# Optimization experiments

Measured on AMD Instinct MI355X. Metric: run time of the kernel, lower is better.

The kernel has to match this reference:

```python
import jax, jax.numpy as jnp
import numpy as np

DIM, DIM_K, DIM_U, HEADS, SCOPE = 256, 16, 1, 4, 23
DIM_V = DIM // HEADS  # 64
EPS = 1e-5


def _bn(x, gamma, beta):
    # training-mode BatchNorm2d over (b, h, w), biased variance, per-channel affine
    mean = jnp.mean(x, axis=(0, 2, 3), keepdims=True)
    var = jnp.var(x, axis=(0, 2, 3), keepdims=True)
    xhat = (x - mean) * jax.lax.rsqrt(var + EPS)
    return xhat * gamma[None, :, None, None] + beta[None, :, None, None]


def setup_inputs() -> dict:
    key = jax.random.key(0)
    ks = jax.random.split(key, 8)
    c_out = HEADS * DIM_K + DIM_K * DIM_U + DIM_V * DIM_U  # 144
    x = jax.random.normal(ks[0], (16, DIM, 64, 64), dtype=jnp.float32)
    w_qkv = jax.random.normal(ks[1], (c_out, DIM), dtype=jnp.float32) * (1.0 / np.sqrt(DIM))
    gamma_q = jnp.ones((HEADS * DIM_K,), jnp.float32)
    beta_q = jnp.zeros((HEADS * DIM_K,), jnp.float32)
    gamma_v = jnp.ones((DIM_V * DIM_U,), jnp.float32)
    beta_v = jnp.zeros((DIM_V * DIM_U,), jnp.float32)
    fan_in = DIM_U * SCOPE * SCOPE
    w_lconv = jax.random.normal(ks[2], (DIM_K, DIM_U, 1, SCOPE, SCOPE), dtype=jnp.float32) * (1.0 / np.sqrt(fan_in))
    b_lconv = jnp.zeros((DIM_K,), jnp.float32)
    return {"x": x, "w_qkv": w_qkv, "gamma_q": gamma_q, "beta_q": beta_q,
            "gamma_v": gamma_v, "beta_v": beta_v, "w_lconv": w_lconv, "b_lconv": b_lconv}


def reference(x, w_qkv, gamma_q, beta_q, gamma_v, beta_v, w_lconv, b_lconv):
    b, c, h, w = x.shape
    m = h * w
    # 1x1 conv projection
    qkv = jnp.einsum('oc,bchw->bohw', w_qkv, x)
    q = qkv[:, :HEADS * DIM_K]
    k = qkv[:, HEADS * DIM_K:HEADS * DIM_K + DIM_K * DIM_U]
    v = qkv[:, HEADS * DIM_K + DIM_K * DIM_U:]
    # q: 'b (k n) h w -> b n k m'
    q = _bn(q, gamma_q, beta_q).reshape(b, DIM_K, HEADS, m).transpose(0, 2, 1, 3)
    # v: 'b (v u) h w -> b u v m'
    v = _bn(v, gamma_v, beta_v).reshape(b, DIM_V, DIM_U, m).transpose(0, 2, 1, 3)
    # k: 'b (u k) h w -> b u k m', softmax over m
    k = jax.nn.softmax(k.reshape(b, DIM_U, DIM_K, m), axis=-1)
    content_lambda = jnp.einsum('bukm,buvm->bkv', k, v)
    # position lambda: Conv3d over (v, h, w) with kernel (1, scope, scope)
    v5 = v.reshape(b, DIM_U, DIM_V, h, w)
    pad = (SCOPE - 1) // 2
    pl = jax.lax.conv_general_dilated(
        v5, w_lconv, window_strides=(1, 1, 1),
        padding=[(0, 0), (pad, pad), (pad, pad)],
        dimension_numbers=('NCDHW', 'OIDHW', 'NCDHW'))
    pl = pl + b_lconv[None, :, None, None, None]
    position_lambda = pl.reshape(b, DIM_K, DIM_V, m)
    content_output = jnp.einsum('bnkm,bkv->bnvm', q, content_lambda)
    position_output = jnp.einsum('bnkm,bkvm->bnvm', q, position_lambda)
    out = (content_output + position_output).reshape(b, HEADS * DIM_V, h, w)
    return out
```

## Files before the change

### kernel.cpp

```cpp
#include <hip/hip_runtime.h>
#include <math.h>

#define NB    16
#define CDIM  256
#define COUT  144
#define MPIX  4096
#define SCOPE 23
#define PADH  11
#define BNEPS 1e-5f

typedef __attribute__((ext_vector_type(4))) float f32x4;
typedef __attribute__((ext_vector_type(8))) short s16x8;

__device__ __forceinline__ unsigned short f2bf(float f) {
    unsigned u = __builtin_bit_cast(unsigned, f);
    unsigned r = (u + 0x7FFFu + ((u >> 16) & 1u)) >> 16;
    return (unsigned short)r;
}

__global__ void prep_frags(const float* __restrict__ w, const float* __restrict__ wl,
                           short* __restrict__ wqf, short* __restrict__ wfrag) {
    int i = blockIdx.x * 256 + threadIdx.x;
    if (i < 36864) {
        int j = i & 7, lane = (i >> 3) & 63;
        int fi = i >> 9;
        int mf = fi % 9, kc = fi / 9;
        int o = mf * 16 + (lane & 15);
        int c = kc * 32 + (lane >> 4) * 8 + j;
        wqf[i] = (short)f2bf(w[o * 256 + c]);
        return;
    }
    int i2 = i - 36864;
    if (i2 < 23 * 64 * 8) {
        int j = i2 & 7, l = (i2 >> 3) & 63, dy = i2 >> 9;
        int k = l & 15, t = ((l >> 4) << 3) + j;
        float wv = (t < SCOPE) ? wl[k * 529 + dy * 23 + t] : 0.f;
        wfrag[i2] = (short)f2bf(wv);
    }
}

__global__ void __launch_bounds__(256, 4) gemm_qkv(const float* __restrict__ x,
                                                   const short* __restrict__ wqf,
                                                   float* __restrict__ qkv,
                                                   float* __restrict__ statpart,
                                                   float* __restrict__ kpart) {
    __shared__ unsigned pk[16 * 65];
    __shared__ float ssum[4][144], ssq[4][144];
    __shared__ float sse[4][16];
    int mt = blockIdx.x, b = blockIdx.y;
    int m0 = mt * 64;
    int tid = threadIdx.x;
    int px64 = tid & 63, c2b = tid >> 6;
    int lane = tid & 63, wv = tid >> 6;
    int pxl = lane & 15, kgq = lane >> 4;
    const float* xb = x + (size_t)b * CDIM * MPIX;
    float* qtb = qkv + (size_t)b * COUT * MPIX;
    const s16x8* wfv = (const s16x8*)wqf;

    f32x4 acc[9];
#pragma unroll
    for (int mf = 0; mf < 9; mf++) acc[mf] = 0.f;

#pragma unroll 1
    for (int kc = 0; kc < 8; kc++) {
        if (kc > 0) __syncthreads();
#pragma unroll
        for (int it = 0; it < 4; it++) {
            int c2 = c2b + it * 4;
            float x0 = xb[(size_t)(kc * 32 + 2 * c2) * MPIX + m0 + px64];
            float x1 = xb[(size_t)(kc * 32 + 2 * c2 + 1) * MPIX + m0 + px64];
            pk[c2 * 65 + px64] = (unsigned)f2bf(x0) | ((unsigned)f2bf(x1) << 16);
        }
        __syncthreads();
        const unsigned* bp = &pk[kgq * 4 * 65 + wv * 16 + pxl];
        int4 bi = make_int4(bp[0], bp[65], bp[130], bp[195]);
        s16x8 bf = __builtin_bit_cast(s16x8, bi);
#pragma unroll
        for (int mf = 0; mf < 9; mf++) {
            s16x8 af = wfv[(kc * 9 + mf) * 64 + lane];
            acc[mf] = __builtin_amdgcn_mfma_f32_16x16x32_bf16(af, bf, acc[mf], 0, 0, 0);
        }
    }

    int m = m0 + wv * 16 + pxl;
#pragma unroll
    for (int mf = 0; mf < 9; mf++) {
#pragma unroll
        for (int r = 0; r < 4; r++) {
            int o = mf * 16 + kgq * 4 + r;
            if (mf < 4) qtb[(size_t)m * 64 + o] = acc[mf][r];
            else qkv[((size_t)b * COUT + o) * MPIX + m] = acc[mf][r];
        }
    }

#pragma unroll
    for (int mf = 0; mf < 9; mf++) {
#pragma unroll
        for (int r = 0; r < 4; r++) {
            float s = acc[mf][r];
            float s2 = s * s;
#pragma unroll
            for (int off = 1; off < 16; off <<= 1) {
                s += __shfl_xor(s, off);
                s2 += __shfl_xor(s2, off);
            }
            if (mf == 4) {
                float e = __expf(acc[mf][r]);
#pragma unroll
                for (int off = 1; off < 16; off <<= 1) e += __shfl_xor(e, off);
                if (pxl == 0) sse[wv][kgq * 4 + r] = e;
            }
            if (pxl == 0) {
                int ch = mf * 16 + kgq * 4 + r;
                ssum[wv][ch] = s;
                ssq[wv][ch] = s2;
            }
        }
    }
    __syncthreads();
    if (tid < 144) {
        float s = ssum[0][tid] + ssum[1][tid] + ssum[2][tid] + ssum[3][tid];
        float s2 = ssq[0][tid] + ssq[1][tid] + ssq[2][tid] + ssq[3][tid];
        size_t idx = (((size_t)tid * 16 + b) * 64 + mt) * 2;
        statpart[idx + 0] = s;
        statpart[idx + 1] = s2;
    }
    if (tid >= 144 && tid < 160) {
        int kc = tid - 144;
        float e = sse[0][kc] + sse[1][kc] + sse[2][kc] + sse[3][kc];
        kpart[((size_t)kc * 16 + b) * 64 + mt] = e;
    }
}

__global__ void stats_finalize(const float* __restrict__ statpart,
                               const float* __restrict__ kpart,
                               const float* __restrict__ gq, const float* __restrict__ bq,
                               const float* __restrict__ gv, const float* __restrict__ bv,
                               float* __restrict__ ascale, float* __restrict__ dshift,
                               float* __restrict__ ksm) {
    int tid = threadIdx.x;
    if (blockIdx.x >= 128) {
        int id = blockIdx.x - 128;
        if (tid < 64) {
            float s = kpart[(size_t)id * 64 + tid];
#pragma unroll
            for (int off = 32; off > 0; off >>= 1) s += __shfl_down(s, off);
            if (tid == 0) ksm[id] = 1.0f / s;
        }
        return;
    }
    int sch = blockIdx.x;
    int gch = (sch < 64) ? sch : sch + 16;
    const float* sp = statpart + (size_t)gch * 1024 * 2;
    float s = 0.f, s2 = 0.f;
    for (int i = tid; i < 1024; i += 256) {
        s += sp[i * 2 + 0];
        s2 += sp[i * 2 + 1];
    }
#pragma unroll
    for (int off = 32; off > 0; off >>= 1) {
        s += __shfl_down(s, off);
        s2 += __shfl_down(s2, off);
    }
    __shared__ float red[8];
    int wid = tid >> 6, lane = tid & 63;
    if (lane == 0) { red[wid * 2] = s; red[wid * 2 + 1] = s2; }
    __syncthreads();
    if (tid == 0) {
        float ts = 0.f, ts2 = 0.f;
#pragma unroll
        for (int w2 = 0; w2 < 4; w2++) { ts += red[w2 * 2]; ts2 += red[w2 * 2 + 1]; }
        const float invN = 1.0f / 65536.0f;
        float mean = ts * invN;
        float var = ts2 * invN - mean * mean;
        float g = (sch < 64) ? gq[sch] : gv[sch - 64];
        float be = (sch < 64) ? bq[sch] : bv[sch - 64];
        float a = g * rsqrtf(var + BNEPS);
        ascale[sch] = a;
        dshift[sch] = be - mean * a;
    }
}

__global__ void cl_partial(const float* __restrict__ qkv, const float* __restrict__ ksm,
                           const float* __restrict__ ascale, const float* __restrict__ dshift,
                           float* __restrict__ clpart) {
    __shared__ float vsT[128][65];
    __shared__ float pk2[16][132];
    __shared__ float skr[16];
    int mc = blockIdx.x, b = blockIdx.y;
    int m0 = mc * 256;
    int tid = threadIdx.x;
    int vc = tid & 63, kg = tid >> 6;
    if (tid < 16) skr[tid] = ksm[(size_t)tid * 16 + b];
    float acc[4] = {0.f, 0.f, 0.f, 0.f};
    for (int half = 0; half < 2; half++) {
        int mh = m0 + half * 128;
        __syncthreads();
        for (int i = tid; i < 64 * 128; i += 256) {
            int r = i >> 7, c = i & 127;
            vsT[c][r] = fmaf(ascale[64 + r], qkv[((size_t)b * COUT + 80 + r) * MPIX + mh + c],
                             dshift[64 + r]);
        }
        for (int i = tid; i < 16 * 128; i += 256) {
            int kc = i >> 7, mm = i & 127;
            pk2[kc][mm] = __expf(qkv[((size_t)b * COUT + 64 + kc) * MPIX + mh + mm]) * skr[kc];
        }
        __syncthreads();
        for (int mm = 0; mm < 128; mm++) {
            float vv = vsT[mm][vc];
#pragma unroll
            for (int i = 0; i < 4; i++) {
                int kc = kg * 4 + i;
                acc[i] = fmaf(pk2[kc][mm], vv, acc[i]);
            }
        }
    }
#pragma unroll
    for (int i = 0; i < 4; i++) {
        int kc = kg * 4 + i;
        clpart[(((size_t)b * 16 + mc) * 16 + kc) * 64 + vc] = acc[i];
    }
}

__global__ void cl_reduce(const float* __restrict__ clpart, float* __restrict__ cl) {
    int b = blockIdx.x;
    for (int o = threadIdx.x; o < 1024; o += 256) {
        float s = 0.f;
        for (int mc = 0; mc < 16; mc++)
            s += clpart[((size_t)b * 16 + mc) * 1024 + o];
        cl[(size_t)b * 1024 + o] = s;
    }
}

__global__ void __launch_bounds__(256) bnq_t(float* __restrict__ qkv,
                                             const float* __restrict__ ascale,
                                             const float* __restrict__ dshift) {
    __shared__ float sv[64][65];
    int mt = blockIdx.x, b = blockIdx.y;
    int m0 = mt * 64;
    float* qb = qkv + (size_t)b * COUT * MPIX;
    int tid = threadIdx.x;
    int c = tid & 63, mg = tid >> 6;
    float a = ascale[c], d = dshift[c];
#pragma unroll
    for (int i = 0; i < 16; i++) {
        int m = mg * 16 + i;
        sv[m][c] = fmaf(a, qb[(size_t)(m0 + m) * 64 + c], d);
    }
    __syncthreads();
    int m = tid >> 2, jb = (tid & 3) * 8;
    unsigned dw[8];
#pragma unroll
    for (int j = 0; j < 8; j++) {
        int cc = jb * 2 + 2 * j;
        dw[j] = (unsigned)f2bf(sv[m][cc]) | ((unsigned)f2bf(sv[m][cc + 1]) << 16);
    }
    unsigned* dst = (unsigned*)qb + (size_t)(m0 + m) * 64 + jb;
    *(uint4*)dst = make_uint4(dw[0], dw[1], dw[2], dw[3]);
    *(uint4*)(dst + 4) = make_uint4(dw[4], dw[5], dw[6], dw[7]);
}

#define SPW 88
#define LD_FRAG(P) __builtin_bit_cast(s16x8, make_int4((P)[0], (P)[2], (P)[4], (P)[6]))
#define STEP(DY, J) do {                                                        \
    const unsigned* pnew_ = xbase + ((DY) + 3) * SPW;                           \
    rw[((J) + 3) & 3][0] = LD_FRAG(pnew_);                                      \
    rw[((J) + 3) & 3][1] = LD_FRAG(pnew_ + 16);                                 \
    int dyn_ = ((DY) + 3 < 22) ? (DY) + 3 : 22;                                 \
    wr[((J) + 3) & 3] = wf[dyn_ * 64 + lane];                                   \
    _Pragma("unroll")                                                           \
    for (int ty_ = 0; ty_ < 4; ty_++) {                                         \
      _Pragma("unroll")                                                         \
      for (int x2_ = 0; x2_ < 2; x2_++) {                                       \
        int t_ = ty_ * 2 + x2_;                                                 \
        acc[t_] = __builtin_amdgcn_mfma_f32_16x16x32_bf16(                      \
            wr[(J) & 3], rw[((J) + ty_) & 3][x2_], acc[t_], 0, 0, 0);           \
      }                                                                         \
    }                                                                           \
  } while (0)

__global__ void __launch_bounds__(256, 4) lambda_main(
    const float* __restrict__ qkv, const float* __restrict__ ascale,
    const float* __restrict__ dshift, const float* __restrict__ cl,
    const short* __restrict__ wfrag, const float* __restrict__ bl,
    float* __restrict__ out) {
    __shared__ unsigned spack[54 * SPW + 8];
    __shared__ float sck[16];

    int vc = blockIdx.x, b = blockIdx.y, h = blockIdx.z;
    int tid = threadIdx.x;

    if (tid < 16) sck[tid] = cl[((size_t)b * 16 + tid) * 64 + vc] + bl[tid];

    float av = ascale[64 + vc], dv = dshift[64 + vc];
    const float* vrow = qkv + ((size_t)b * COUT + 80 + vc) * MPIX;
    for (int i = tid; i < 54 * SPW; i += 256) {
        int y = i / SPW, e = i - y * SPW;
        int iy = h * 32 + y - PADH;
        float f0 = 0.f, f1 = 0.f;
        if ((unsigned)iy < 64u) {
            int ix0 = e - PADH, ix1 = e - PADH + 1;
            if ((unsigned)ix0 < 64u) f0 = fmaf(av, vrow[iy * 64 + ix0], dv);
            if ((unsigned)ix1 < 64u) f1 = fmaf(av, vrow[iy * 64 + ix1], dv);
        }
        spack[i] = (unsigned)f2bf(f0) | ((unsigned)f2bf(f1) << 16);
    }
    if (tid < 8) spack[54 * SPW + tid] = 0u;
    __syncthreads();

    int lane = tid & 63;
    int wv = tid >> 6;
    int px = lane & 15;
    int kg = lane >> 4;
    const s16x8* wf = (const s16x8*)wfrag;

    const unsigned* qtb = (const unsigned*)(qkv + (size_t)b * COUT * MPIX);
    float* ob = out + (size_t)b * 256 * MPIX;

    float sck_l[4];
#pragma unroll
    for (int r = 0; r < 4; r++) sck_l[r] = sck[kg * 4 + r];

#pragma unroll 1
    for (int gg = 0; gg < 2; gg++) {
        int y0 = (gg * 4 + wv) * 4;
        const unsigned* base = &spack[y0 * SPW + px + kg * 8];

#pragma unroll 1
        for (int xh = 0; xh < 2; xh++) {
            const unsigned* xbase = base + xh * 32;
            f32x4 acc[8];
#pragma unroll
            for (int t = 0; t < 8; t++) acc[t] = 0.f;

            s16x8 rw[4][2];
            s16x8 wr[4];
#pragma unroll
            for (int r0 = 0; r0 < 3; r0++) {
                const unsigned* p = xbase + r0 * SPW;
                rw[r0][0] = LD_FRAG(p);
                rw[r0][1] = LD_FRAG(p + 16);
            }
#pragma unroll
            for (int s = 0; s < 3; s++) wr[s] = wf[s * 64 + lane];

#pragma unroll 1
            for (int i8 = 0; i8 < 2; i8++) {
                int dyb = i8 * 8;
                STEP(dyb + 0, 0);
                STEP(dyb + 1, 1);
                STEP(dyb + 2, 2);
                STEP(dyb + 3, 3);
                STEP(dyb + 4, 4);
                STEP(dyb + 5, 5);
                STEP(dyb + 6, 6);
                STEP(dyb + 7, 7);
            }
            STEP(16, 0);
            STEP(17, 1);
            STEP(18, 2);
            STEP(19, 3);
            STEP(20, 4);
            STEP(21, 5);
            STEP(22, 6);

#pragma unroll
            for (int t = 0; t < 8; t++) {
                int ty = t >> 1, x2 = t & 1;
                int m0 = (h * 32 + y0 + ty) * 64 + (xh * 2 + x2) * 16;
                float lam[4];
#pragma unroll
                for (int r = 0; r < 4; r++) lam[r] = acc[t][r] + sck_l[r];
                const unsigned* qp = &qtb[(size_t)(m0 + px) * 64 + kg * 8];
                uint4 qa = *(const uint4*)qp;
                uint4 qb4 = *(const uint4*)(qp + 4);
                unsigned dws[8] = {qa.x, qa.y, qa.z, qa.w, qb4.x, qb4.y, qb4.z, qb4.w};
                float po[4] = {0.f, 0.f, 0.f, 0.f};
#pragma unroll
                for (int d = 0; d < 8; d++) {
                    float q0 = __builtin_bit_cast(float, dws[d] << 16);
                    float q1 = __builtin_bit_cast(float, dws[d] & 0xffff0000u);
                    int i0 = 2 * d, i1 = 2 * d + 1;
                    po[i0 & 3] = fmaf(q0, lam[i0 >> 2], po[i0 & 3]);
                    po[i1 & 3] = fmaf(q1, lam[i1 >> 2], po[i1 & 3]);
                }
#pragma unroll
                for (int n = 0; n < 4; n++) {
                    po[n] += __shfl_xor(po[n], 16);
                    po[n] += __shfl_xor(po[n], 32);
                }
                float sv = (kg == 0) ? po[0] : (kg == 1) ? po[1] : (kg == 2) ? po[2] : po[3];
                ob[(size_t)(kg * 64 + vc) * MPIX + m0 + px] = sv;
            }
        }
    }
}

extern "C" void kernel_launch(void* const* d_in, const int* in_sizes, int n_in,
                              void* d_out, int out_size, void* d_ws, size_t ws_size,
                              hipStream_t stream) {
    const float* x      = (const float*)d_in[0];
    const float* w_qkv  = (const float*)d_in[1];
    const float* gq     = (const float*)d_in[2];
    const float* bq     = (const float*)d_in[3];
    const float* gv     = (const float*)d_in[4];
    const float* bv     = (const float*)d_in[5];
    const float* wl     = (const float*)d_in[6];
    const float* bl     = (const float*)d_in[7];
    float* out = (float*)d_out;

    float* ws     = (float*)d_ws;
    float* qkv    = ws;
    float* ascale = qkv + 9437184;
    float* dshift = ascale + 128;
    float* clpart = dshift + 128;
    float* clb    = clpart + 262144;
    short* wfrag  = (short*)(clb + 16384);
    short* wqf    = (short*)(clb + 16384 + 5888 + 64);
    float* statpart = (float*)(wqf + 36864);
    float* kpart  = statpart + 294912;
    float* ksm    = kpart + 16384;

    prep_frags<<<190, 256, 0, stream>>>(w_qkv, wl, wqf, wfrag);
    gemm_qkv<<<dim3(64, 16), 256, 0, stream>>>(x, wqf, qkv, statpart, kpart);
    stats_finalize<<<384, 256, 0, stream>>>(statpart, kpart, gq, bq, gv, bv,
                                            ascale, dshift, ksm);
    cl_partial<<<dim3(16, 16), 256, 0, stream>>>(qkv, ksm, ascale, dshift, clpart);
    cl_reduce<<<16, 256, 0, stream>>>(clpart, clb);
    bnq_t<<<dim3(64, 16), 256, 0, stream>>>(qkv, ascale, dshift);
    lambda_main<<<dim3(64, 16, 2), 256, 0, stream>>>(qkv, ascale, dshift, clb, wfrag, bl, out);
}
```

Before: 200.6 us.

## Merge content-lambda partials and q transform into one launch, fold reduce into main

Combines the cl_partial and bnq_t kernels into a single launch whose blocks take one of two roles by blockIdx.x, so the two independent jobs run concurrently. It also removes the cl_reduce kernel by having lambda_main sum the 16 partials directly when it loads the content lambda. This cuts two kernel launches and their serialization gaps. In exchange, each lambda_main block does a small redundant 16-way reduction, and the smem footprint for the q-transform blocks is now the larger union size.

```diff
diff --git a/kernel.cpp b/kernel.cpp
--- a/kernel.cpp
+++ b/kernel.cpp
@@ -181,15 +181,46 @@
     }
 }
 
-__global__ void cl_partial(const float* __restrict__ qkv, const float* __restrict__ ksm,
-                           const float* __restrict__ ascale, const float* __restrict__ dshift,
-                           float* __restrict__ clpart) {
-    __shared__ float vsT[128][65];
-    __shared__ float pk2[16][132];
-    __shared__ float skr[16];
-    int mc = blockIdx.x, b = blockIdx.y;
+__global__ void __launch_bounds__(256) cl_bnq(float* __restrict__ qkv,
+                                              const float* __restrict__ ksm,
+                                              const float* __restrict__ ascale,
+                                              const float* __restrict__ dshift,
+                                              float* __restrict__ clpart) {
+    __shared__ float smem[128 * 65 + 16 * 132 + 16];
+    int role = blockIdx.x, b = blockIdx.y;
+    int tid = threadIdx.x;
+
+    if (role >= 16) {
+        float (*sv)[65] = (float(*)[65])smem;
+        int mt = role - 16;
+        int m0 = mt * 64;
+        float* qb = qkv + (size_t)b * COUT * MPIX;
+        int c = tid & 63, mg = tid >> 6;
+        float a = ascale[c], d = dshift[c];
+#pragma unroll
+        for (int i = 0; i < 16; i++) {
+            int m = mg * 16 + i;
+            sv[m][c] = fmaf(a, qb[(size_t)(m0 + m) * 64 + c], d);
+        }
+        __syncthreads();
+        int m = tid >> 2, jb = (tid & 3) * 8;
+        unsigned dw[8];
+#pragma unroll
+        for (int j = 0; j < 8; j++) {
+            int cc = jb * 2 + 2 * j;
+            dw[j] = (unsigned)f2bf(sv[m][cc]) | ((unsigned)f2bf(sv[m][cc + 1]) << 16);
+        }
+        unsigned* dst = (unsigned*)qb + (size_t)(m0 + m) * 64 + jb;
+        *(uint4*)dst = make_uint4(dw[0], dw[1], dw[2], dw[3]);
+        *(uint4*)(dst + 4) = make_uint4(dw[4], dw[5], dw[6], dw[7]);
+        return;
+    }
+
+    float (*vsT)[65] = (float(*)[65])smem;
+    float (*pk2)[132] = (float(*)[132])(smem + 128 * 65);
+    float* skr = smem + 128 * 65 + 16 * 132;
+    int mc = role;
     int m0 = mc * 256;
-    int tid = threadIdx.x;
     int vc = tid & 63, kg = tid >> 6;
     if (tid < 16) skr[tid] = ksm[(size_t)tid * 16 + b];
     float acc[4] = {0.f, 0.f, 0.f, 0.f};
@@ -220,44 +251,6 @@
         int kc = kg * 4 + i;
         clpart[(((size_t)b * 16 + mc) * 16 + kc) * 64 + vc] = acc[i];
     }
-}
-
-__global__ void cl_reduce(const float* __restrict__ clpart, float* __restrict__ cl) {
-    int b = blockIdx.x;
-    for (int o = threadIdx.x; o < 1024; o += 256) {
-        float s = 0.f;
-        for (int mc = 0; mc < 16; mc++)
-            s += clpart[((size_t)b * 16 + mc) * 1024 + o];
-        cl[(size_t)b * 1024 + o] = s;
-    }
-}
-
-__global__ void __launch_bounds__(256) bnq_t(float* __restrict__ qkv,
-                                             const float* __restrict__ ascale,
-                                             const float* __restrict__ dshift) {
-    __shared__ float sv[64][65];
-    int mt = blockIdx.x, b = blockIdx.y;
-    int m0 = mt * 64;
-    float* qb = qkv + (size_t)b * COUT * MPIX;
-    int tid = threadIdx.x;
-    int c = tid & 63, mg = tid >> 6;
-    float a = ascale[c], d = dshift[c];
-#pragma unroll
-    for (int i = 0; i < 16; i++) {
-        int m = mg * 16 + i;
-        sv[m][c] = fmaf(a, qb[(size_t)(m0 + m) * 64 + c], d);
-    }
-    __syncthreads();
-    int m = tid >> 2, jb = (tid & 3) * 8;
-    unsigned dw[8];
-#pragma unroll
-    for (int j = 0; j < 8; j++) {
-        int cc = jb * 2 + 2 * j;
-        dw[j] = (unsigned)f2bf(sv[m][cc]) | ((unsigned)f2bf(sv[m][cc + 1]) << 16);
-    }
-    unsigned* dst = (unsigned*)qb + (size_t)(m0 + m) * 64 + jb;
-    *(uint4*)dst = make_uint4(dw[0], dw[1], dw[2], dw[3]);
-    *(uint4*)(dst + 4) = make_uint4(dw[4], dw[5], dw[6], dw[7]);
 }
 
 #define SPW 88
@@ -281,7 +274,7 @@
 
 __global__ void __launch_bounds__(256, 4) lambda_main(
     const float* __restrict__ qkv, const float* __restrict__ ascale,
-    const float* __restrict__ dshift, const float* __restrict__ cl,
+    const float* __restrict__ dshift, const float* __restrict__ clpart,
     const short* __restrict__ wfrag, const float* __restrict__ bl,
     float* __restrict__ out) {
     __shared__ unsigned spack[54 * SPW + 8];
@@ -290,7 +283,12 @@
     int vc = blockIdx.x, b = blockIdx.y, h = blockIdx.z;
     int tid = threadIdx.x;
 
-    if (tid < 16) sck[tid] = cl[((size_t)b * 16 + tid) * 64 + vc] + bl[tid];
+    if (tid < 16) {
+        float s = 0.f;
+        for (int mc2 = 0; mc2 < 16; mc2++)
+            s += clpart[(((size_t)b * 16 + mc2) * 16 + tid) * 64 + vc];
+        sck[tid] = s + bl[tid];
+    }
 
     float av = ascale[64 + vc], dv = dshift[64 + vc];
     const float* vrow = qkv + ((size_t)b * COUT + 80 + vc) * MPIX;
@@ -414,9 +412,8 @@
     float* ascale = qkv + 9437184;
     float* dshift = ascale + 128;
     float* clpart = dshift + 128;
-    float* clb    = clpart + 262144;
-    short* wfrag  = (short*)(clb + 16384);
-    short* wqf    = (short*)(clb + 16384 + 5888 + 64);
+    short* wfrag  = (short*)(clpart + 262144);
+    short* wqf    = (short*)(clpart + 262144 + 5888 + 64);
     float* statpart = (float*)(wqf + 36864);
     float* kpart  = statpart + 294912;
     float* ksm    = kpart + 16384;
@@ -425,8 +422,6 @@
     gemm_qkv<<<dim3(64, 16), 256, 0, stream>>>(x, wqf, qkv, statpart, kpart);
     stats_finalize<<<384, 256, 0, stream>>>(statpart, kpart, gq, bq, gv, bv,
                                             ascale, dshift, ksm);
-    cl_partial<<<dim3(16, 16), 256, 0, stream>>>(qkv, ksm, ascale, dshift, clpart);
-    cl_reduce<<<16, 256, 0, stream>>>(clpart, clb);
-    bnq_t<<<dim3(64, 16), 256, 0, stream>>>(qkv, ascale, dshift);
-    lambda_main<<<dim3(64, 16, 2), 256, 0, stream>>>(qkv, ascale, dshift, clb, wfrag, bl, out);
-}
+    cl_bnq<<<dim3(80, 16), 256, 0, stream>>>(qkv, ksm, ascale, dshift, clpart);
+    lambda_main<<<dim3(64, 16, 2), 256, 0, stream>>>(qkv, ascale, dshift, clpart, wfrag, bl, out);
+}
```

Result: faster. 192.9 us (-3.8%).
